# Kernel tuning notes

Measured on AMD Instinct MI355X. Metric: run time of the kernel, lower is better.

## Reference

```python
import math
import jax, jax.numpy as jnp
import numpy as np

B, T, D = 4, 2048, 1024
H, DH = 16, 64
FF = 4096
EPS = 1e-5


def setup_inputs() -> dict:
    key = jax.random.key(0)
    ks = jax.random.split(key, 12)
    s = 0.02
    inp = {
        "x": jax.random.normal(ks[0], (B, T, D), dtype=jnp.float32),
        "ln1_g": jnp.ones((D,), jnp.float32),
        "ln1_b": jnp.zeros((D,), jnp.float32),
        "ln2_g": jnp.ones((D,), jnp.float32),
        "ln2_b": jnp.zeros((D,), jnp.float32),
        # torch nn.Linear convention: weight shape [out, in], y = x @ W.T + b
        "wq": jax.random.normal(ks[1], (D, D), jnp.float32) * s,
        "bq": jnp.zeros((D,), jnp.float32),
        "wk": jax.random.normal(ks[2], (D, D), jnp.float32) * s,
        "bk": jnp.zeros((D,), jnp.float32),
        "wv": jax.random.normal(ks[3], (D, D), jnp.float32) * s,
        "bv": jnp.zeros((D,), jnp.float32),
        "wo": jax.random.normal(ks[4], (D, D), jnp.float32) * s,
        "bo": jnp.zeros((D,), jnp.float32),
        "w1": jax.random.normal(ks[5], (FF, D), jnp.float32) * s,
        "b1": jnp.zeros((FF,), jnp.float32),
        "w2": jax.random.normal(ks[6], (D, FF), jnp.float32) * s,
        "b2": jnp.zeros((D,), jnp.float32),
    }
    return inp


def _layernorm(h, g, b):
    mu = jnp.mean(h, axis=-1, keepdims=True)
    var = jnp.mean(jnp.square(h - mu), axis=-1, keepdims=True)
    return (h - mu) * jax.lax.rsqrt(var + EPS) * g + b


def _block(x, ln1_g, ln1_b, ln2_g, ln2_b, wq, bq, wk, bk, wv, bv, wo, bo, w1, b1, w2, b2):
    b, t, d = x.shape
    h = _layernorm(x, ln1_g, ln1_b)
    q = (h @ wq.T + bq).reshape(b, t, H, DH)
    k = (h @ wk.T + bk).reshape(b, t, H, DH)
    v = (h @ wv.T + bv).reshape(b, t, H, DH)
    # full (non-causal) attention, as in the torch module
    att = jnp.einsum("bqhd,bkhd->bhqk", q, k) / math.sqrt(DH)
    att = jax.nn.softmax(att, axis=-1)
    out = jnp.einsum("bhqk,bkhd->bqhd", att, v).reshape(b, t, d)
    x = x + (out @ wo.T + bo)
    h2 = _layernorm(x, ln2_g, ln2_b)
    ff = jax.nn.gelu(h2 @ w1.T + b1, approximate=False) @ w2.T + b2
    return x + ff


def reference(x, ln1_g, ln1_b, ln2_g, ln2_b, wq, bq, wk, bk, wv, bv, wo, bo, w1, b1, w2, b2):
    return _block(x, ln1_g, ln1_b, ln2_g, ln2_b, wq, bq, wk, bk, wv, bv, wo, bo, w1, b1, w2, b2)
```

## Files before the change

### kernel.cpp

```cpp
#include <hip/hip_runtime.h>
#include <cstdint>
#include <cstddef>

typedef __attribute__((ext_vector_type(8))) __bf16 bf16x8;
typedef __attribute__((ext_vector_type(4))) float f32x4;
typedef __attribute__((ext_vector_type(8))) unsigned short us8;
typedef __attribute__((ext_vector_type(4))) unsigned short us4;

__device__ inline unsigned short f2bf(float f) {
    unsigned int u = __float_as_uint(f);
    u += 0x7fffu + ((u >> 16) & 1u);
    return (unsigned short)(u >> 16);
}

__device__ inline unsigned int pkbf_t(float hi, float lo) {
    return __builtin_amdgcn_perm(__float_as_uint(hi), __float_as_uint(lo), 0x07060302u);
}

__device__ inline void async_copy16(const void* g, void* l) {
    __builtin_amdgcn_global_load_lds(
        (const __attribute__((address_space(1))) unsigned int*)g,
        (__attribute__((address_space(3))) unsigned int*)l, 16, 0, 0);
}

__global__ __launch_bounds__(256) void cvt_bf16(const float* __restrict__ in,
                                                unsigned short* __restrict__ out, int n4) {
    int i = blockIdx.x * 256 + threadIdx.x;
    if (i < n4) {
        float4 v = ((const float4*)in)[i];
        us4 o;
        o[0] = f2bf(v.x); o[1] = f2bf(v.y); o[2] = f2bf(v.z); o[3] = f2bf(v.w);
        ((us4*)out)[i] = o;
    }
}

__global__ __launch_bounds__(256) void ln_bf16(const float* __restrict__ X,
                                               const float* __restrict__ g,
                                               const float* __restrict__ b,
                                               unsigned short* __restrict__ out) {
    int row = blockIdx.x;
    int t = threadIdx.x;
    float4 v = ((const float4*)(X + (size_t)row * 1024))[t];
    float s  = v.x + v.y + v.z + v.w;
    float s2 = v.x * v.x + v.y * v.y + v.z * v.z + v.w * v.w;
#pragma unroll
    for (int m = 1; m < 64; m <<= 1) {
        s  += __shfl_xor(s, m, 64);
        s2 += __shfl_xor(s2, m, 64);
    }
    __shared__ float red[8];
    int w = t >> 6, l = t & 63;
    if (l == 0) { red[w] = s; red[4 + w] = s2; }
    __syncthreads();
    s  = red[0] + red[1] + red[2] + red[3];
    s2 = red[4] + red[5] + red[6] + red[7];
    float mu  = s * (1.0f / 1024.0f);
    float var = s2 * (1.0f / 1024.0f) - mu * mu;
    float rs  = rsqrtf(var + 1e-5f);
    int c = t * 4;
    float4 gv = *(const float4*)(g + c);
    float4 bv = *(const float4*)(b + c);
    us4 o;
    o[0] = f2bf((v.x - mu) * rs * gv.x + bv.x);
    o[1] = f2bf((v.y - mu) * rs * gv.y + bv.y);
    o[2] = f2bf((v.z - mu) * rs * gv.z + bv.z);
    o[3] = f2bf((v.w - mu) * rs * gv.w + bv.w);
    *(us4*)(out + (size_t)row * 1024 + c) = o;
}

#define BM 128
#define BN 128
#define BK 32

template <int EPI>
__global__ __launch_bounds__(256) void gemm_nt(const unsigned short* __restrict__ A,
                                               const unsigned short* __restrict__ B,
                                               const float* __restrict__ bias,
                                               const float* __restrict__ resid,
                                               void* __restrict__ Cout, int N, int K) {
    __shared__ __align__(16) unsigned short As[BM * BK];
    __shared__ __align__(16) unsigned short Bs[BN * BK];
    const int tid = threadIdx.x;
    const int lane = tid & 63, w = tid >> 6;
    const int quad = lane >> 4, l16 = lane & 15;
    const int wr = w >> 1, wc = w & 1;
    const size_t bm = (size_t)blockIdx.y * BM;
    const size_t bn = (size_t)blockIdx.x * BN;

    f32x4 acc[4][4];
#pragma unroll
    for (int i = 0; i < 4; i++)
#pragma unroll
        for (int j = 0; j < 4; j++) acc[i][j] = (f32x4){0.f, 0.f, 0.f, 0.f};

    for (int k0 = 0; k0 < K; k0 += BK) {
#pragma unroll
        for (int i = 0; i < 2; i++) {
            int e = (i * 256 + tid) * 8;
            int r = e >> 5, c = e & 31;
            async_copy16(A + (bm + r) * K + k0 + c, &As[e]);
            async_copy16(B + (bn + r) * K + k0 + c, &Bs[e]);
        }
        __syncthreads();
        bf16x8 af[4], bfr[4];
#pragma unroll
        for (int mt = 0; mt < 4; mt++)
            af[mt] = *(const bf16x8*)&As[(wr * 64 + mt * 16 + l16) * BK + quad * 8];
#pragma unroll
        for (int nt = 0; nt < 4; nt++)
            bfr[nt] = *(const bf16x8*)&Bs[(wc * 64 + nt * 16 + l16) * BK + quad * 8];
#pragma unroll
        for (int mt = 0; mt < 4; mt++)
#pragma unroll
            for (int nt = 0; nt < 4; nt++)
                acc[mt][nt] = __builtin_amdgcn_mfma_f32_16x16x32_bf16(af[mt], bfr[nt],
                                                                      acc[mt][nt], 0, 0, 0);
        __syncthreads();
    }

#pragma unroll
    for (int mt = 0; mt < 4; mt++) {
#pragma unroll
        for (int nt = 0; nt < 4; nt++) {
#pragma unroll
            for (int r = 0; r < 4; r++) {
                size_t row = bm + wr * 64 + mt * 16 + quad * 4 + r;
                size_t col = bn + wc * 64 + nt * 16 + l16;
                float v = acc[mt][nt][r] + bias[col];
                if (EPI == 1) {
                    v = 0.5f * v * (1.0f + erff(v * 0.70710678118654752f));
                    ((unsigned short*)Cout)[row * N + col] = f2bf(v);
                } else if (EPI == 2) {
                    ((float*)Cout)[row * N + col] = v + resid[row * N + col];
                } else if (EPI == 6) {
                    int sel = (int)(bn >> 10);
                    if (sel == 0) {
                        ((unsigned short*)Cout)[row * 1024 + col] =
                            f2bf(v * 0.18033688011112042f);
                    } else {
                        int key = (int)row & 2047;
                        int bh  = (((int)row >> 11) << 4) | (((int)col >> 6) & 15);
                        int dh  = (int)col & 63;
                        size_t addr;
                        if (sel == 1)
                            addr = 8388608 + (size_t)bh * 131072 +
                                   (size_t)(key >> 6) * 4096 + (size_t)(key & 63) * 64 +
                                   ((((dh >> 3) ^ (key & 7))) << 3) + (dh & 7);
                        else
                            addr = 16777216 + (size_t)bh * 131072 +
                                   (size_t)(key >> 6) * 4096 + (size_t)dh * 64 +
                                   (((((key >> 3) & 7) ^ (dh & 7))) << 3) + (key & 7);
                        ((unsigned short*)Cout)[addr] = f2bf(v);
                    }
                }
            }
        }
    }
}

__global__ __launch_bounds__(256) void attn_kernel(const unsigned short* __restrict__ Q,
                                                   const unsigned short* __restrict__ Kb,
                                                   const unsigned short* __restrict__ Vtb,
                                                   unsigned short* __restrict__ O) {
    const int bh   = blockIdx.x >> 4;
    const int qblk = blockIdx.x & 15;
    const int b = bh >> 4, h = bh & 15;
    const int tid = threadIdx.x, lane = tid & 63, w = tid >> 6;
    const int quad = lane >> 4, l16 = lane & 15;
    const int sw = l16 & 7;

    __shared__ __align__(16) unsigned short smem[16384];
    unsigned short* Ks  = smem;
    unsigned short* Vts = smem + 4096;
    unsigned short* Psw = smem + 8192 + w * 2048;

    const size_t qrow0 = (size_t)b * 2048 + (size_t)qblk * 128 + w * 32;
    const int hcol = h * 64;

    bf16x8 qfr[2][2];
#pragma unroll
    for (int qf = 0; qf < 2; qf++)
#pragma unroll
        for (int kp = 0; kp < 2; kp++)
            qfr[qf][kp] = *(const bf16x8*)(Q + (qrow0 + qf * 16 + l16) * 1024 +
                                           hcol + kp * 32 + quad * 8);

    f32x4 acc[4][2];
#pragma unroll
    for (int df = 0; df < 4; df++)
#pragma unroll
        for (int qf = 0; qf < 2; qf++) acc[df][qf] = (f32x4){0.f, 0.f, 0.f, 0.f};
    float l_[2] = {0.f, 0.f};

    const unsigned short* ksrc = Kb  + (size_t)bh * 131072;
    const unsigned short* vsrc = Vtb + (size_t)bh * 131072;

    for (int kt = 0; kt < 32; ++kt) {
        __syncthreads();
        const unsigned short* kg = ksrc + kt * 4096;
        const unsigned short* vg = vsrc + kt * 4096;
        async_copy16(kg + tid * 8,        &Ks[tid * 8]);
        async_copy16(kg + 2048 + tid * 8, &Ks[2048 + tid * 8]);
        async_copy16(vg + tid * 8,        &Vts[tid * 8]);
        async_copy16(vg + 2048 + tid * 8, &Vts[2048 + tid * 8]);
        __syncthreads();

        f32x4 s[4][2];
#pragma unroll
        for (int mf = 0; mf < 4; mf++)
#pragma unroll
            for (int qf = 0; qf < 2; qf++) s[mf][qf] = (f32x4){0.f, 0.f, 0.f, 0.f};
#pragma unroll
        for (int kp = 0; kp < 2; kp++) {
#pragma unroll
            for (int mf = 0; mf < 4; mf++) {
                bf16x8 kf = *(const bf16x8*)&Ks[(mf * 16 + l16) * 64 +
                                                (((kp * 4 + quad) ^ sw) << 3)];
#pragma unroll
                for (int qf = 0; qf < 2; qf++)
                    s[mf][qf] = __builtin_amdgcn_mfma_f32_16x16x32_bf16(kf, qfr[qf][kp],
                                                                        s[mf][qf], 0, 0, 0);
            }
        }

#pragma unroll
        for (int mf = 0; mf < 4; mf++)
#pragma unroll
            for (int qf = 0; qf < 2; qf++) {
                float e0 = exp2f(s[mf][qf][0]);
                float e1 = exp2f(s[mf][qf][1]);
                float e2 = exp2f(s[mf][qf][2]);
                float e3 = exp2f(s[mf][qf][3]);
                l_[qf] += (e0 + e1) + (e2 + e3);
                *(uint2*)&Psw[(qf * 16 + l16) * 64 +
                              (((mf * 2 + (quad >> 1)) ^ sw) << 3) + ((quad & 1) << 2)] =
                    make_uint2(pkbf_t(e1, e0), pkbf_t(e3, e2));
            }
        asm volatile("s_waitcnt lgkmcnt(0)" ::: "memory");

#pragma unroll
        for (int kp = 0; kp < 2; kp++) {
            bf16x8 pf[2];
#pragma unroll
            for (int qf = 0; qf < 2; qf++)
                pf[qf] = *(const bf16x8*)&Psw[(qf * 16 + l16) * 64 +
                                              (((kp * 4 + quad) ^ sw) << 3)];
#pragma unroll
            for (int df = 0; df < 4; df++) {
                bf16x8 vf = *(const bf16x8*)&Vts[(df * 16 + l16) * 64 +
                                                 (((kp * 4 + quad) ^ sw) << 3)];
#pragma unroll
                for (int qf = 0; qf < 2; qf++)
                    acc[df][qf] = __builtin_amdgcn_mfma_f32_16x16x32_bf16(vf, pf[qf],
                                                                          acc[df][qf], 0, 0, 0);
            }
        }
    }

#pragma unroll
    for (int qf = 0; qf < 2; qf++) {
        l_[qf] += __shfl_xor(l_[qf], 16, 64);
        l_[qf] += __shfl_xor(l_[qf], 32, 64);
    }

    __syncthreads();
    float inv[2] = {1.f / l_[0], 1.f / l_[1]};
    unsigned short* Ls = smem;
#pragma unroll
    for (int df = 0; df < 4; df++)
#pragma unroll
        for (int qf = 0; qf < 2; qf++)
#pragma unroll
            for (int r = 0; r < 4; r++) {
                int dh = df * 16 + quad * 4 + r;
                int q  = w * 32 + qf * 16 + l16;
                Ls[dh * 130 + q] =
                    (unsigned short)((__float_as_uint(acc[df][qf][r] * inv[qf]) + 0x8000u) >> 16);
            }
    __syncthreads();
    int q = tid >> 1, dh0 = (tid & 1) * 32;
    size_t obase = ((size_t)b * 2048 + (size_t)qblk * 128 + q) * 1024 + hcol + dh0;
#pragma unroll
    for (int c = 0; c < 4; c++) {
        us8 o;
#pragma unroll
        for (int j = 0; j < 8; j++) o[j] = Ls[(dh0 + c * 8 + j) * 130 + q];
        *(us8*)(O + obase + c * 8) = o;
    }
}

extern "C" void kernel_launch(void* const* d_in, const int* in_sizes, int n_in,
                              void* d_out, int out_size, void* d_ws, size_t ws_size,
                              hipStream_t stream) {
    const float* x     = (const float*)d_in[0];
    const float* ln1_g = (const float*)d_in[1];
    const float* ln1_b = (const float*)d_in[2];
    const float* ln2_g = (const float*)d_in[3];
    const float* ln2_b = (const float*)d_in[4];
    const float* wq = (const float*)d_in[5];
    const float* bq = (const float*)d_in[6];
    const float* wk = (const float*)d_in[7];
    const float* bk = (const float*)d_in[8];
    const float* wv = (const float*)d_in[9];
    const float* bv = (const float*)d_in[10];
    const float* wo = (const float*)d_in[11];
    const float* bo = (const float*)d_in[12];
    const float* w1 = (const float*)d_in[13];
    const float* b1 = (const float*)d_in[14];
    const float* w2 = (const float*)d_in[15];
    const float* b2 = (const float*)d_in[16];

    const size_t MB = 1u << 20;
    char* ws = (char*)d_ws;
    unsigned short* wqkvb = (unsigned short*)(ws + 0 * MB);
    unsigned short* wob  = (unsigned short*)(ws + 6 * MB);
    unsigned short* w1b  = (unsigned short*)(ws + 8 * MB);
    unsigned short* w2b  = (unsigned short*)(ws + 16 * MB);
    unsigned short* hb   = (unsigned short*)(ws + 24 * MB);
    unsigned short* qkvb = (unsigned short*)(ws + 40 * MB);
    unsigned short* qb   = qkvb;
    unsigned short* kblk = qkvb + 8388608;
    unsigned short* vtblk= qkvb + 16777216;
    float*          x1   = (float*)(ws + 56 * MB);
    unsigned short* h2b  = (unsigned short*)(ws + 40 * MB);
    unsigned short* ff1b = (unsigned short*)(ws + 88 * MB);
    float*          bqkv = (float*)(ws + 151 * MB);

    const int D = 1024, FF = 4096, Mrows = 8192;

    cvt_bf16<<<(D * D / 4 + 255) / 256, 256, 0, stream>>>(wq, wqkvb,               D * D / 4);
    cvt_bf16<<<(D * D / 4 + 255) / 256, 256, 0, stream>>>(wk, wqkvb + D * D,       D * D / 4);
    cvt_bf16<<<(D * D / 4 + 255) / 256, 256, 0, stream>>>(wv, wqkvb + 2 * D * D,   D * D / 4);
    cvt_bf16<<<(D * D / 4 + 255) / 256, 256, 0, stream>>>(wo, wob, D * D / 4);
    cvt_bf16<<<(FF * D / 4 + 255) / 256, 256, 0, stream>>>(w1, w1b, FF * D / 4);
    cvt_bf16<<<(FF * D / 4 + 255) / 256, 256, 0, stream>>>(w2, w2b, FF * D / 4);

    hipMemcpyAsync(bqkv,            bq, D * sizeof(float), hipMemcpyDeviceToDevice, stream);
    hipMemcpyAsync(bqkv + D,        bk, D * sizeof(float), hipMemcpyDeviceToDevice, stream);
    hipMemcpyAsync(bqkv + 2 * D,    bv, D * sizeof(float), hipMemcpyDeviceToDevice, stream);

    ln_bf16<<<Mrows, 256, 0, stream>>>(x, ln1_g, ln1_b, hb);

    dim3 gQKV(3 * D / BN, Mrows / BM);
    gemm_nt<6><<<gQKV, 256, 0, stream>>>(hb, wqkvb, bqkv, nullptr, qkvb, D, D);

    attn_kernel<<<1024, 256, 0, stream>>>(qb, kblk, vtblk, hb);

    dim3 gD(D / BN, Mrows / BM);
    gemm_nt<2><<<gD, 256, 0, stream>>>(hb, wob, bo, x, x1, D, D);

    ln_bf16<<<Mrows, 256, 0, stream>>>(x1, ln2_g, ln2_b, h2b);

    dim3 gFF(FF / BN, Mrows / BM);
    gemm_nt<1><<<gFF, 256, 0, stream>>>(h2b, w1b, b1, nullptr, ff1b, FF, D);

    gemm_nt<2><<<gD, 256, 0, stream>>>(ff1b, w2b, b2, x1, (float*)d_out, D, FF);
}
```

Baseline: 640.9 us.

## Double-buffer K tiles and prefetch next K/V during attention compute

Adds a second K buffer in shared memory and issues the async global-to-LDS copy for the next K tile before computing the current QK^T. The next V tile is loaded right after the PV MFMAs. Explicit vmcnt waits and raw s_barrier replace the two __syncthreads per iteration, so load latency can overlap compute. It also raises wave priority around the MFMA sections. Shared memory grows, which may lower occupancy, and correctness depends on the hand-counted vmcnt values.

```diff
diff --git a/kernel.cpp b/kernel.cpp
--- a/kernel.cpp
+++ b/kernel.cpp
@@ -169,10 +169,9 @@
     const int quad = lane >> 4, l16 = lane & 15;
     const int sw = l16 & 7;
 
-    __shared__ __align__(16) unsigned short smem[16384];
-    unsigned short* Ks  = smem;
-    unsigned short* Vts = smem + 4096;
-    unsigned short* Psw = smem + 8192 + w * 2048;
+    __shared__ __align__(16) unsigned short smem[20480];
+    unsigned short* Vts = smem + 8192;
+    unsigned short* Psw = smem + 12288 + w * 2048;
 
     const size_t qrow0 = (size_t)b * 2048 + (size_t)qblk * 128 + w * 32;
     const int hcol = h * 64;
@@ -185,6 +184,14 @@
             qfr[qf][kp] = *(const bf16x8*)(Q + (qrow0 + qf * 16 + l16) * 1024 +
                                            hcol + kp * 32 + quad * 8);
 
+    const unsigned short* ksrc = Kb  + (size_t)bh * 131072;
+    const unsigned short* vsrc = Vtb + (size_t)bh * 131072;
+
+    async_copy16(ksrc + tid * 8,        smem + tid * 8);
+    async_copy16(ksrc + 2048 + tid * 8, smem + 2048 + tid * 8);
+    async_copy16(vsrc + tid * 8,        Vts + tid * 8);
+    async_copy16(vsrc + 2048 + tid * 8, Vts + 2048 + tid * 8);
+
     f32x4 acc[4][2];
 #pragma unroll
     for (int df = 0; df < 4; df++)
@@ -192,24 +199,25 @@
         for (int qf = 0; qf < 2; qf++) acc[df][qf] = (f32x4){0.f, 0.f, 0.f, 0.f};
     float l_[2] = {0.f, 0.f};
 
-    const unsigned short* ksrc = Kb  + (size_t)bh * 131072;
-    const unsigned short* vsrc = Vtb + (size_t)bh * 131072;
-
     for (int kt = 0; kt < 32; ++kt) {
-        __syncthreads();
-        const unsigned short* kg = ksrc + kt * 4096;
-        const unsigned short* vg = vsrc + kt * 4096;
-        async_copy16(kg + tid * 8,        &Ks[tid * 8]);
-        async_copy16(kg + 2048 + tid * 8, &Ks[2048 + tid * 8]);
-        async_copy16(vg + tid * 8,        &Vts[tid * 8]);
-        async_copy16(vg + 2048 + tid * 8, &Vts[2048 + tid * 8]);
-        __syncthreads();
+        unsigned short* Ks = (kt & 1) ? (smem + 4096) : smem;
+        if (kt < 31) {
+            unsigned short* Kd = (kt & 1) ? smem : (smem + 4096);
+            const unsigned short* kg = ksrc + (size_t)(kt + 1) * 4096;
+            async_copy16(kg + tid * 8,        Kd + tid * 8);
+            async_copy16(kg + 2048 + tid * 8, Kd + 2048 + tid * 8);
+            asm volatile("s_waitcnt vmcnt(4)" ::: "memory");
+        } else {
+            asm volatile("s_waitcnt vmcnt(2)" ::: "memory");
+        }
+        asm volatile("s_barrier" ::: "memory");
 
         f32x4 s[4][2];
 #pragma unroll
         for (int mf = 0; mf < 4; mf++)
 #pragma unroll
             for (int qf = 0; qf < 2; qf++) s[mf][qf] = (f32x4){0.f, 0.f, 0.f, 0.f};
+        __builtin_amdgcn_s_setprio(1);
 #pragma unroll
         for (int kp = 0; kp < 2; kp++) {
 #pragma unroll
@@ -222,6 +230,7 @@
                                                                         s[mf][qf], 0, 0, 0);
             }
         }
+        __builtin_amdgcn_s_setprio(0);
 
 #pragma unroll
         for (int mf = 0; mf < 4; mf++)
@@ -238,6 +247,14 @@
             }
         asm volatile("s_waitcnt lgkmcnt(0)" ::: "memory");
 
+        if (kt < 31) {
+            asm volatile("s_waitcnt vmcnt(2)" ::: "memory");
+        } else {
+            asm volatile("s_waitcnt vmcnt(0)" ::: "memory");
+        }
+        asm volatile("s_barrier" ::: "memory");
+
+        __builtin_amdgcn_s_setprio(1);
 #pragma unroll
         for (int kp = 0; kp < 2; kp++) {
             bf16x8 pf[2];
@@ -254,6 +271,14 @@
                     acc[df][qf] = __builtin_amdgcn_mfma_f32_16x16x32_bf16(vf, pf[qf],
                                                                           acc[df][qf], 0, 0, 0);
             }
+        }
+        __builtin_amdgcn_s_setprio(0);
+
+        asm volatile("s_barrier" ::: "memory");
+        if (kt < 31) {
+            const unsigned short* vg = vsrc + (size_t)(kt + 1) * 4096;
+            async_copy16(vg + tid * 8,        Vts + tid * 8);
+            async_copy16(vg + 2048 + tid * 8, Vts + 2048 + tid * 8);
         }
     }
 
```

Result: no change. 634.3 us (-1.0%).
